# Kernel tuning notes

Hardware: AMD Instinct MI355X
Metric: run time of the kernel (lower is better)

The kernel has to match this reference:

```python
import jax, jax.numpy as jnp
import numpy as np

NUM_PRODUCTS = 100000
NUM_CATEGORIES = 1000
P_DIM = 64          # product embedding dim
C_DIM = P_DIM // 2  # 32
T_DIM = P_DIM // 4  # 16
U_DIM = P_DIM // 4  # 16
HID = 128
B, S, L = 1024, 50, 20


def setup_inputs() -> dict:
    key = jax.random.key(0)
    ks = jax.random.split(key, 24)
    inp = {}
    inp['product_input'] = jax.random.randint(ks[0], (B, S, L), 1, NUM_PRODUCTS + 1, dtype=jnp.int32)
    inp['categories_input'] = jax.random.randint(ks[1], (B, S, L), 1, NUM_CATEGORIES + 1, dtype=jnp.int32)
    inp['user_age_input'] = jax.random.uniform(ks[2], (B,), jnp.float32) * 80.0
    inp['user_timestamps_input'] = jax.random.uniform(ks[3], (B, S), jnp.float32)
    inp['user_gender_input'] = jax.random.randint(ks[4], (B,), 0, 2).astype(jnp.float32)
    # embedding tables (padding_idx=0 -> zero row)
    emb_p = jax.random.normal(ks[5], (NUM_PRODUCTS + 1, P_DIM), jnp.float32) * 0.02
    inp['emb_p'] = emb_p.at[0].set(0.0)
    emb_c = jax.random.normal(ks[6], (NUM_CATEGORIES + 1, C_DIM), jnp.float32) * 0.02
    inp['emb_c'] = emb_c.at[0].set(0.0)
    # small linears
    inp['W_ts'] = jax.random.normal(ks[7], (T_DIM, 1), jnp.float32) * 0.1
    inp['b_ts'] = jnp.zeros((T_DIM,), jnp.float32)
    inp['W_uf'] = jax.random.normal(ks[8], (U_DIM, 2), jnp.float32) * 0.1
    inp['b_uf'] = jnp.zeros((U_DIM,), jnp.float32)
    # 2-layer LSTM params (torch layout: [4H, in], gate order i,f,g,o)
    IN = P_DIM + C_DIM + T_DIM + U_DIM  # 128
    sc = 1.0 / np.sqrt(HID)
    inp['W_ih0'] = jax.random.uniform(ks[9], (4 * HID, IN), jnp.float32, -sc, sc)
    inp['W_hh0'] = jax.random.uniform(ks[10], (4 * HID, HID), jnp.float32, -sc, sc)
    inp['b_ih0'] = jax.random.uniform(ks[11], (4 * HID,), jnp.float32, -sc, sc)
    inp['b_hh0'] = jax.random.uniform(ks[12], (4 * HID,), jnp.float32, -sc, sc)
    inp['W_ih1'] = jax.random.uniform(ks[13], (4 * HID, HID), jnp.float32, -sc, sc)
    inp['W_hh1'] = jax.random.uniform(ks[14], (4 * HID, HID), jnp.float32, -sc, sc)
    inp['b_ih1'] = jax.random.uniform(ks[15], (4 * HID,), jnp.float32, -sc, sc)
    inp['b_hh1'] = jax.random.uniform(ks[16], (4 * HID,), jnp.float32, -sc, sc)
    # MLP head
    inp['W1'] = jax.random.normal(ks[17], (HID // 2, HID), jnp.float32) * 0.05
    inp['b1'] = jnp.zeros((HID // 2,), jnp.float32)
    inp['W2'] = jax.random.normal(ks[18], (NUM_PRODUCTS + 1, HID // 2), jnp.float32) * 0.05
    inp['b2'] = jnp.zeros((NUM_PRODUCTS + 1,), jnp.float32)
    return inp


def _lstm_layer(x, Wih, Whh, bih, bhh):
    # x: [S, B, D] -> outputs [S, B, H], final h [B, H]
    Bb = x.shape[1]
    h0 = jnp.zeros((Bb, HID), x.dtype)
    def step(carry, xt):
        h, c = carry
        gates = xt @ Wih.T + bih + h @ Whh.T + bhh
        i, f, g, o = jnp.split(gates, 4, axis=-1)
        c = jax.nn.sigmoid(f) * c + jax.nn.sigmoid(i) * jnp.tanh(g)
        h = jax.nn.sigmoid(o) * jnp.tanh(c)
        return (h, c), h
    (h, c), ys = jax.lax.scan(step, (h0, h0), x)
    return ys, h


def reference(product_input, categories_input, user_age_input, user_timestamps_input,
              user_gender_input, emb_p, emb_c, W_ts, b_ts, W_uf, b_uf,
              W_ih0, W_hh0, b_ih0, b_hh0, W_ih1, W_hh1, b_ih1, b_hh1,
              W1, b1, W2, b2):
    # per-basket mean-pooled embeddings (fused gather + segment mean)
    prod = emb_p[product_input].mean(axis=2)          # [B, S, 64]
    cat = emb_c[categories_input].mean(axis=2)        # [B, S, 32]
    ts = user_timestamps_input[..., None] @ W_ts.T + b_ts  # [B, S, 16]
    uf = jnp.stack([user_age_input, user_gender_input], axis=1) @ W_uf.T + b_uf  # [B, 16]
    uf = jnp.broadcast_to(uf[:, None, :], (uf.shape[0], prod.shape[1], uf.shape[1]))
    x = jnp.concatenate([prod, cat, ts, uf], axis=-1)  # [B, S, 128]
    x = jnp.transpose(x, (1, 0, 2))                    # [S, B, 128]
    ys0, _ = _lstm_layer(x, W_ih0, W_hh0, b_ih0, b_hh0)
    _, h_last = _lstm_layer(ys0, W_ih1, W_hh1, b_ih1, b_hh1)  # [B, H]
    # dropout is identity in eval mode
    hidden = jax.nn.relu(h_last @ W1.T + b1)
    logits = hidden @ W2.T + b2                        # [B, num_products+1]
    return logits
```

## Files before the change

### kernel.cpp

```cpp
#include <hip/hip_runtime.h>

#define B_    1024
#define S_    50
#define L_    20
#define NOUT  100001

typedef __attribute__((ext_vector_type(8))) short bh8;
typedef __attribute__((ext_vector_type(4))) float fx4;

__device__ __forceinline__ unsigned short f2bf(float x){
  unsigned u = __float_as_uint(x);
  unsigned r = (u + 0x7FFFu + ((u >> 16) & 1u)) >> 16;
  return (unsigned short)r;
}
__device__ __forceinline__ float bf2f(unsigned short h){
  return __uint_as_float(((unsigned)h) << 16);
}
__device__ __forceinline__ float sigm(float x){
  return __builtin_amdgcn_rcpf(1.f + __expf(-x));
}
__device__ __forceinline__ float tanh_(float x){
  return 1.f - 2.f*__builtin_amdgcn_rcpf(__expf(2.f*x) + 1.f);
}

__device__ __forceinline__ void frag_convert_row(const float* src, bh8& hv, bh8& lv){
  #pragma unroll
  for (int j = 0; j < 8; j++){
    float x = src[j];
    unsigned short hb = f2bf(x);
    hv[j] = (short)hb;
    lv[j] = (short)f2bf(x - bf2f(hb));
  }
}

__global__ __launch_bounds__(256) void prep_lstm_w(
    const float* __restrict__ Wih0, const float* __restrict__ Whh0,
    const float* __restrict__ bih0, const float* __restrict__ bhh0,
    const float* __restrict__ Wih1, const float* __restrict__ Whh1,
    const float* __restrict__ bih1, const float* __restrict__ bhh1,
    short* __restrict__ wsw, float* __restrict__ wsbias){
  int tid = blockIdx.x*256 + threadIdx.x;
  if (tid < 1024){
    int l = tid >> 9, n = tid & 511;
    wsbias[l*512 + n] = l ? (bih1[n] + bhh1[n]) : (bih0[n] + bhh0[n]);
  }
  if (tid >= 32768) return;
  int lane = tid & 63;
  int kt   = (tid >> 6) & 7;
  int nt   = (tid >> 9) & 31;
  int l    = tid >> 14;
  const float* Wih = l ? Wih1 : Wih0;
  const float* Whh = l ? Whh1 : Whh0;
  int n = nt*16 + (lane & 15);
  int kbase = kt*32 + (lane >> 4)*8;
  size_t base = ((((size_t)l*32 + nt)*8 + kt)*64 + lane)*8;
  for (int j = 0; j < 8; j++){
    int k = kbase + j;
    float w = (k < 128) ? Wih[n*128 + k] : Whh[n*128 + (k - 128)];
    wsw[base + j] = (short)f2bf(w);
  }
}

__global__ __launch_bounds__(256) void prep_w2(const float* __restrict__ W2,
                                               short* __restrict__ out){
  long i = (long)blockIdx.x*256 + threadIdx.x;
  if (i >= 100016L*64) return;
  long row = i >> 6;
  float v = (row < NOUT) ? W2[i] : 0.f;
  out[i] = (short)f2bf(v);
}

__global__ __launch_bounds__(256) void features(
    const int* __restrict__ pidx, const int* __restrict__ cidx,
    const float* __restrict__ age, const float* __restrict__ ts,
    const float* __restrict__ gender,
    const float* __restrict__ embp, const float* __restrict__ embc,
    const float* __restrict__ Wts, const float* __restrict__ bts,
    const float* __restrict__ Wuf, const float* __restrict__ bufv,
    short* __restrict__ xfrag){
  const int bx = blockIdx.x;
  const int bt = bx & 63, s = bx >> 6;
  const int b0 = bt*16;
  const int tid = threadIdx.x;
  __shared__ int pi[320], ci[320];
  __shared__ __align__(16) float XF[16][132];
  for (int i = tid; i < 640; i += 256){
    if (i < 320){
      int row = i/20, l = i - row*20;
      pi[i] = pidx[((size_t)(b0+row)*S_ + s)*L_ + l];
    } else {
      int j = i - 320;
      int row = j/20, l = j - row*20;
      ci[j] = cidx[((size_t)(b0+row)*S_ + s)*L_ + l];
    }
  }
  __syncthreads();
  const int m = tid >> 4, fg = tid & 15;
  float a[8];
  if (fg < 8){
    int f0 = fg*8;
    float4 s0 = {0,0,0,0}, s1 = {0,0,0,0};
    for (int l = 0; l < L_; l++){
      const float4* p = (const float4*)(embp + (size_t)pi[m*20+l]*64 + f0);
      float4 u = p[0], v = p[1];
      s0.x += u.x; s0.y += u.y; s0.z += u.z; s0.w += u.w;
      s1.x += v.x; s1.y += v.y; s1.z += v.z; s1.w += v.w;
    }
    a[0]=s0.x*0.05f; a[1]=s0.y*0.05f; a[2]=s0.z*0.05f; a[3]=s0.w*0.05f;
    a[4]=s1.x*0.05f; a[5]=s1.y*0.05f; a[6]=s1.z*0.05f; a[7]=s1.w*0.05f;
  } else if (fg < 12){
    int f0 = (fg-8)*8;
    float4 s0 = {0,0,0,0}, s1 = {0,0,0,0};
    for (int l = 0; l < L_; l++){
      const float4* p = (const float4*)(embc + (size_t)ci[m*20+l]*32 + f0);
      float4 u = p[0], v = p[1];
      s0.x += u.x; s0.y += u.y; s0.z += u.z; s0.w += u.w;
      s1.x += v.x; s1.y += v.y; s1.z += v.z; s1.w += v.w;
    }
    a[0]=s0.x*0.05f; a[1]=s0.y*0.05f; a[2]=s0.z*0.05f; a[3]=s0.w*0.05f;
    a[4]=s1.x*0.05f; a[5]=s1.y*0.05f; a[6]=s1.z*0.05f; a[7]=s1.w*0.05f;
  } else if (fg < 14){
    int j0 = (fg-12)*8;
    float tv = ts[(size_t)(b0+m)*S_ + s];
    #pragma unroll
    for (int e = 0; e < 8; e++) a[e] = tv*Wts[j0+e] + bts[j0+e];
  } else {
    int j0 = (fg-14)*8;
    float av = age[b0+m], gv = gender[b0+m];
    #pragma unroll
    for (int e = 0; e < 8; e++){
      int j = j0+e;
      a[e] = av*Wuf[2*j] + gv*Wuf[2*j+1] + bufv[j];
    }
  }
  {
    int f0 = fg*8;
    *(float4*)&XF[m][f0]   = (float4){a[0],a[1],a[2],a[3]};
    *(float4*)&XF[m][f0+4] = (float4){a[4],a[5],a[6],a[7]};
  }
  __syncthreads();
  const int kt = tid >> 6, ls = tid & 63;
  const int mm = ls & 15, a2 = ls >> 4;
  bh8 hv, lv;
  frag_convert_row(&XF[mm][kt*32 + a2*8], hv, lv);
  size_t ob = ((((size_t)s*64 + bt)*2 + 0)*4 + kt)*512 + (size_t)ls*8;
  *(bh8*)(xfrag + ob)        = hv;
  *(bh8*)(xfrag + ob + 2048) = lv;
}

__global__ __launch_bounds__(512, 2) void lstm_kernel(
    const short* __restrict__ xfrag, const short* __restrict__ wsw,
    const float* __restrict__ wsbias,
    const float* __restrict__ W1, const float* __restrict__ b1,
    short* __restrict__ hidden_bf){
  __shared__ __align__(16) short XAhi[2][2048], XAlo[2][2048];
  __shared__ __align__(16) short H0hi[2][2048], H0lo[2][2048];
  __shared__ __align__(16) short H1hi[2][2048], H1lo[2][2048];
  __shared__ __align__(16) float XH0f[16][132], XH1f[16][132];
  const int tid  = threadIdx.x;
  const int w    = tid >> 6, lane = tid & 63;
  const int col  = lane & 15, quad = lane >> 4;
  const int bt   = blockIdx.x;
  const int u    = w & 3;
  const bool t1  = (w >= 4);
  const int lsel = t1 ? 1 : 0;
  const int plane = tid >> 8, sl = tid & 255;
  const bh8* wp = (const bh8*)wsw;

  for (int idx = tid; idx < 2048; idx += 512){
    H0hi[1][idx] = 0; H0lo[1][idx] = 0;
    H1hi[0][idx] = 0; H1lo[0][idx] = 0;
  }
  float bz[2][4];
  #pragma unroll
  for (int ss = 0; ss < 2; ss++)
    #pragma unroll
    for (int g = 0; g < 4; g++)
      bz[ss][g] = wsbias[lsel*512 + (g*8 + 2*u + ss)*16 + col];
  float cst[2][4] = {{0,0,0,0},{0,0,0,0}};
  {
    float4 v = *(const float4*)(xfrag + ((size_t)bt*2 + plane)*2048 + (size_t)sl*8);
    *(float4*)((plane ? XAlo[0] : XAhi[0]) + sl*8) = v;
  }
  __syncthreads();

  for (int i = 0; i <= S_; i++){
    const int cb = i & 1, pb = cb ^ 1;
    int tp = (i+1 < S_) ? i+1 : S_-1;
    float4 pf = *(const float4*)(xfrag + (((size_t)tp*64 + bt)*2 + plane)*2048 + (size_t)sl*8);

    const bool act = t1 ? (i >= 1) : (i < S_);
    if (act){
      fx4 acc[2][4];
      #pragma unroll
      for (int ss = 0; ss < 2; ss++)
        #pragma unroll
        for (int g = 0; g < 4; g++)
          acc[ss][g] = (fx4){bz[ss][g], bz[ss][g], bz[ss][g], bz[ss][g]};
      #pragma unroll
      for (int kt = 0; kt < 8; kt++){
        const short* ph;
        const short* pl;
        if (!t1){
          ph = (kt < 4) ? &XAhi[cb][kt*512 + lane*8] : &H0hi[pb][(kt-4)*512 + lane*8];
          pl = (kt < 4) ? &XAlo[cb][kt*512 + lane*8] : &H0lo[pb][(kt-4)*512 + lane*8];
        } else {
          ph = (kt < 4) ? &H0hi[pb][kt*512 + lane*8] : &H1hi[pb][(kt-4)*512 + lane*8];
          pl = (kt < 4) ? &H0lo[pb][kt*512 + lane*8] : &H1lo[pb][(kt-4)*512 + lane*8];
        }
        bh8 ah = *(const bh8*)ph;
        bh8 al = *(const bh8*)pl;
        #pragma unroll
        for (int ss = 0; ss < 2; ss++)
          #pragma unroll
          for (int g = 0; g < 4; g++){
            bh8 bb = wp[(size_t)((lsel*32 + g*8 + 2*u + ss)*8 + kt)*64 + lane];
            acc[ss][g] = __builtin_amdgcn_mfma_f32_16x16x32_bf16(ah, bb, acc[ss][g], 0, 0, 0);
            acc[ss][g] = __builtin_amdgcn_mfma_f32_16x16x32_bf16(al, bb, acc[ss][g], 0, 0, 0);
          }
      }
      float (*XH)[132] = t1 ? XH1f : XH0f;
      #pragma unroll
      for (int ss = 0; ss < 2; ss++)
        #pragma unroll
        for (int r = 0; r < 4; r++){
          float cc = sigm(acc[ss][1][r])*cst[ss][r] + sigm(acc[ss][0][r])*tanh_(acc[ss][2][r]);
          cst[ss][r] = cc;
          XH[quad*4 + r][u*32 + ss*16 + col] = sigm(acc[ss][3][r])*tanh_(cc);
        }
      {
        const int mm = lane & 15, a2 = lane >> 4;
        bh8 hv, lv;
        frag_convert_row(&XH[mm][u*32 + a2*8], hv, lv);
        if (!t1){
          *(bh8*)&H0hi[cb][u*512 + lane*8] = hv;
          *(bh8*)&H0lo[cb][u*512 + lane*8] = lv;
        } else {
          *(bh8*)&H1hi[cb][u*512 + lane*8] = hv;
          *(bh8*)&H1lo[cb][u*512 + lane*8] = lv;
        }
      }
    }
    *(float4*)((plane ? XAlo[pb] : XAhi[pb]) + sl*8) = pf;
    __syncthreads();
  }
  #pragma unroll
  for (int e = 0; e < 2; e++){
    int mm2 = (tid >> 6)*2 + e;
    int cc2 = tid & 63;
    float s = b1[cc2];
    #pragma unroll 8
    for (int k = 0; k < 128; k++) s += XH1f[mm2][k]*W1[cc2*128 + k];
    s = fmaxf(s, 0.f);
    hidden_bf[(size_t)(bt*16 + mm2)*64 + cc2] = (short)f2bf(s);
  }
}

__global__ __launch_bounds__(256) void head2(
    const short* __restrict__ hid, const short* __restrict__ w2,
    const float* __restrict__ b2, float* __restrict__ out){
  __shared__ __align__(16) float HS[4][16][132];
  const int tid = threadIdx.x;
  const int w = tid >> 6, lane = tid & 63;
  const int col = lane & 15, quad = lane >> 4;
  const int mt = blockIdx.x & 63;
  const int chunk = blockIdx.x >> 6;
  const bh8* hp = (const bh8*)hid;
  bh8 a0 = hp[(size_t)(mt*16 + col)*8 + quad];
  bh8 a1 = hp[(size_t)(mt*16 + col)*8 + 4 + quad];
  const bh8* wpt = (const bh8*)w2;
  #pragma unroll
  for (int i = 0; i < 8; i++){
    int nt = chunk*32 + w*8 + i;
    if (nt < 6251){
      int n = nt*16 + col;
      bh8 b0v = wpt[(size_t)n*8 + quad];
      bh8 b1v = wpt[(size_t)n*8 + 4 + quad];
      fx4 a = {0.f,0.f,0.f,0.f};
      a = __builtin_amdgcn_mfma_f32_16x16x32_bf16(a0, b0v, a, 0, 0, 0);
      a = __builtin_amdgcn_mfma_f32_16x16x32_bf16(a1, b1v, a, 0, 0, 0);
      float bias = (n < NOUT) ? b2[n] : 0.f;
      #pragma unroll
      for (int r = 0; r < 4; r++) HS[w][quad*4 + r][i*16 + col] = a[r] + bias;
    }
  }
  __syncthreads();
  const long rowbase = (long)mt*16;
  const int n0 = chunk*512 + w*128;
  #pragma unroll
  for (int p = 0; p < 8; p++){
    int row = p*2 + (lane >> 5);
    int c4 = (lane & 31)*4;
    int gc = n0 + c4;
    float4 v = *(const float4*)&HS[w][row][c4];
    if (gc + 3 < NOUT){
      *(float4*)&out[(rowbase + row)*NOUT + gc] = v;
    } else {
      float vv[4] = {v.x, v.y, v.z, v.w};
      #pragma unroll
      for (int k2 = 0; k2 < 4; k2++)
        if (gc + k2 < NOUT) out[(rowbase + row)*NOUT + gc + k2] = vv[k2];
    }
  }
}

extern "C" void kernel_launch(void* const* d_in, const int* in_sizes, int n_in,
                              void* d_out, int out_size, void* d_ws, size_t ws_size,
                              hipStream_t stream){
  const int*   prod = (const int*)  d_in[0];
  const int*   cat  = (const int*)  d_in[1];
  const float* age  = (const float*)d_in[2];
  const float* ts   = (const float*)d_in[3];
  const float* gen  = (const float*)d_in[4];
  const float* embp = (const float*)d_in[5];
  const float* embc = (const float*)d_in[6];
  const float* Wts  = (const float*)d_in[7];
  const float* bts  = (const float*)d_in[8];
  const float* Wuf  = (const float*)d_in[9];
  const float* bufv = (const float*)d_in[10];
  const float* Wih0 = (const float*)d_in[11];
  const float* Whh0 = (const float*)d_in[12];
  const float* bih0 = (const float*)d_in[13];
  const float* bhh0 = (const float*)d_in[14];
  const float* Wih1 = (const float*)d_in[15];
  const float* Whh1 = (const float*)d_in[16];
  const float* bih1 = (const float*)d_in[17];
  const float* bhh1 = (const float*)d_in[18];
  const float* W1   = (const float*)d_in[19];
  const float* b1   = (const float*)d_in[20];
  const float* W2   = (const float*)d_in[21];
  const float* b2   = (const float*)d_in[22];
  float* out = (float*)d_out;

  char* ws = (char*)d_ws;
  short* ws_x    = (short*)(ws);
  short* ws_w    = (short*)(ws + 26214400);
  float* ws_bias = (float*)(ws + 26738688);
  short* ws_hid  = (short*)(ws + 26742784);
  short* ws_w2   = (short*)(ws + 26873856);

  prep_lstm_w<<<128, 256, 0, stream>>>(Wih0, Whh0, bih0, bhh0,
                                       Wih1, Whh1, bih1, bhh1, ws_w, ws_bias);
  prep_w2<<<25004, 256, 0, stream>>>(W2, ws_w2);
  features<<<3200, 256, 0, stream>>>(prod, cat, age, ts, gen, embp, embc,
                                     Wts, bts, Wuf, bufv, ws_x);
  lstm_kernel<<<64, 512, 0, stream>>>(ws_x, ws_w, ws_bias, W1, b1, ws_hid);
  head2<<<196*64, 256, 0, stream>>>(ws_hid, ws_w2, b2, out);
}
```

Baseline: 1.097 ms.

## Double LSTM block to 16 waves, one 16-column gate slice per wave

The LSTM kernel now launches 1024 threads per block instead of 512. Each wave computes one 16-column hidden slice across all four gates, so the two slices per wave become one, halving the serial MFMA chain per wave on the latency-bound recurrent critical path. The h fragment writes are split across lanes by hi/lo phase, and the MFMA loop runs at raised wave priority. In exchange there are more waves per barrier, each wave re-reads the same A fragments from LDS, and the launch-bounds change may affect the register budget.

```diff
diff --git a/kernel.cpp b/kernel.cpp
--- a/kernel.cpp
+++ b/kernel.cpp
@@ -148,7 +148,7 @@
   *(bh8*)(xfrag + ob + 2048) = lv;
 }
 
-__global__ __launch_bounds__(512, 2) void lstm_kernel(
+__global__ __launch_bounds__(1024, 4) void lstm_kernel(
     const short* __restrict__ xfrag, const short* __restrict__ wsw,
     const float* __restrict__ wsbias,
     const float* __restrict__ W1, const float* __restrict__ b1,
@@ -161,42 +161,39 @@
   const int w    = tid >> 6, lane = tid & 63;
   const int col  = lane & 15, quad = lane >> 4;
   const int bt   = blockIdx.x;
-  const int u    = w & 3;
-  const bool t1  = (w >= 4);
+  const int u    = w & 7;
+  const bool t1  = (w >= 8);
   const int lsel = t1 ? 1 : 0;
-  const int plane = tid >> 8, sl = tid & 255;
+  const int pl2  = tid >> 9, sl2 = tid & 511;
   const bh8* wp = (const bh8*)wsw;
 
-  for (int idx = tid; idx < 2048; idx += 512){
+  for (int idx = tid; idx < 2048; idx += 1024){
     H0hi[1][idx] = 0; H0lo[1][idx] = 0;
     H1hi[0][idx] = 0; H1lo[0][idx] = 0;
   }
-  float bz[2][4];
+  float bz[4];
   #pragma unroll
-  for (int ss = 0; ss < 2; ss++)
-    #pragma unroll
-    for (int g = 0; g < 4; g++)
-      bz[ss][g] = wsbias[lsel*512 + (g*8 + 2*u + ss)*16 + col];
-  float cst[2][4] = {{0,0,0,0},{0,0,0,0}};
+  for (int g = 0; g < 4; g++)
+    bz[g] = wsbias[lsel*512 + (g*8 + u)*16 + col];
+  float cst[4] = {0,0,0,0};
   {
-    float4 v = *(const float4*)(xfrag + ((size_t)bt*2 + plane)*2048 + (size_t)sl*8);
-    *(float4*)((plane ? XAlo[0] : XAhi[0]) + sl*8) = v;
+    float2 v = *(const float2*)(xfrag + ((size_t)bt*2 + pl2)*2048 + (size_t)sl2*4);
+    *(float2*)((pl2 ? XAlo[0] : XAhi[0]) + sl2*4) = v;
   }
   __syncthreads();
 
   for (int i = 0; i <= S_; i++){
     const int cb = i & 1, pb = cb ^ 1;
     int tp = (i+1 < S_) ? i+1 : S_-1;
-    float4 pf = *(const float4*)(xfrag + (((size_t)tp*64 + bt)*2 + plane)*2048 + (size_t)sl*8);
+    float2 pf = *(const float2*)(xfrag + (((size_t)tp*64 + bt)*2 + pl2)*2048 + (size_t)sl2*4);
 
     const bool act = t1 ? (i >= 1) : (i < S_);
     if (act){
-      fx4 acc[2][4];
-      #pragma unroll
-      for (int ss = 0; ss < 2; ss++)
-        #pragma unroll
-        for (int g = 0; g < 4; g++)
-          acc[ss][g] = (fx4){bz[ss][g], bz[ss][g], bz[ss][g], bz[ss][g]};
+      fx4 acc[4];
+      #pragma unroll
+      for (int g = 0; g < 4; g++)
+        acc[g] = (fx4){bz[g], bz[g], bz[g], bz[g]};
+      __builtin_amdgcn_s_setprio(1);
       #pragma unroll
       for (int kt = 0; kt < 8; kt++){
         const short* ph;
@@ -211,43 +208,38 @@
         bh8 ah = *(const bh8*)ph;
         bh8 al = *(const bh8*)pl;
         #pragma unroll
-        for (int ss = 0; ss < 2; ss++)
-          #pragma unroll
-          for (int g = 0; g < 4; g++){
-            bh8 bb = wp[(size_t)((lsel*32 + g*8 + 2*u + ss)*8 + kt)*64 + lane];
-            acc[ss][g] = __builtin_amdgcn_mfma_f32_16x16x32_bf16(ah, bb, acc[ss][g], 0, 0, 0);
-            acc[ss][g] = __builtin_amdgcn_mfma_f32_16x16x32_bf16(al, bb, acc[ss][g], 0, 0, 0);
-          }
-      }
-      float (*XH)[132] = t1 ? XH1f : XH0f;
-      #pragma unroll
-      for (int ss = 0; ss < 2; ss++)
-        #pragma unroll
-        for (int r = 0; r < 4; r++){
-          float cc = sigm(acc[ss][1][r])*cst[ss][r] + sigm(acc[ss][0][r])*tanh_(acc[ss][2][r]);
-          cst[ss][r] = cc;
-          XH[quad*4 + r][u*32 + ss*16 + col] = sigm(acc[ss][3][r])*tanh_(cc);
-        }
-      {
-        const int mm = lane & 15, a2 = lane >> 4;
-        bh8 hv, lv;
-        frag_convert_row(&XH[mm][u*32 + a2*8], hv, lv);
-        if (!t1){
-          *(bh8*)&H0hi[cb][u*512 + lane*8] = hv;
-          *(bh8*)&H0lo[cb][u*512 + lane*8] = lv;
-        } else {
-          *(bh8*)&H1hi[cb][u*512 + lane*8] = hv;
-          *(bh8*)&H1lo[cb][u*512 + lane*8] = lv;
+        for (int g = 0; g < 4; g++){
+          bh8 bb = wp[(size_t)((lsel*32 + g*8 + u)*8 + kt)*64 + lane];
+          acc[g] = __builtin_amdgcn_mfma_f32_16x16x32_bf16(ah, bb, acc[g], 0, 0, 0);
+          acc[g] = __builtin_amdgcn_mfma_f32_16x16x32_bf16(al, bb, acc[g], 0, 0, 0);
         }
       }
-    }
-    *(float4*)((plane ? XAlo[pb] : XAhi[pb]) + sl*8) = pf;
+      __builtin_amdgcn_s_setprio(0);
+      float (*XH)[132] = t1 ? XH1f : XH0f;
+      #pragma unroll
+      for (int r = 0; r < 4; r++){
+        float cc = sigm(acc[1][r])*cst[r] + sigm(acc[0][r])*tanh_(acc[2][r]);
+        cst[r] = cc;
+        XH[quad*4 + r][u*16 + col] = sigm(acc[3][r])*tanh_(cc);
+      }
+      {
+        const int mm = lane & 15, qq = (lane >> 4) & 1, phase = lane >> 5;
+        bh8 hv, lv;
+        frag_convert_row(&XH[mm][u*16 + qq*8], hv, lv);
+        const int off = (u >> 1)*512 + ((2*(u & 1) + qq)*16 + mm)*8;
+        short* dsth = t1 ? &H1hi[cb][off] : &H0hi[cb][off];
+        short* dstl = t1 ? &H1lo[cb][off] : &H0lo[cb][off];
+        short* dst  = phase ? dstl : dsth;
+        bh8   val   = phase ? lv : hv;
+        *(bh8*)dst = val;
+      }
+    }
+    *(float2*)((pl2 ? XAlo[pb] : XAhi[pb]) + sl2*4) = pf;
     __syncthreads();
   }
-  #pragma unroll
-  for (int e = 0; e < 2; e++){
-    int mm2 = (tid >> 6)*2 + e;
-    int cc2 = tid & 63;
+  {
+    const int mm2 = tid >> 6;
+    const int cc2 = tid & 63;
     float s = b1[cc2];
     #pragma unroll 8
     for (int k = 0; k < 128; k++) s += XH1f[mm2][k]*W1[cc2*128 + k];
@@ -344,6 +336,6 @@
   prep_w2<<<25004, 256, 0, stream>>>(W2, ws_w2);
   features<<<3200, 256, 0, stream>>>(prod, cat, age, ts, gen, embp, embc,
                                      Wts, bts, Wuf, bufv, ws_x);
-  lstm_kernel<<<64, 512, 0, stream>>>(ws_x, ws_w, ws_bias, W1, b1, ws_hid);
+  lstm_kernel<<<64, 1024, 0, stream>>>(ws_x, ws_w, ws_bias, W1, b1, ws_hid);
   head2<<<196*64, 256, 0, stream>>>(ws_hid, ws_w2, b2, out);
 }
```

Result: faster. 983.5 us (-10.3%).
